# Kernel optimization log

Hardware: AMD Instinct MI355X
Metric: run time of the kernel (lower is better)

The kernel has to match this reference:

```python
import jax, jax.numpy as jnp
import numpy as np

B, T, D_MODEL, H = 2, 2048, 1024, 16
D_HEAD = D_MODEL // H


def setup_inputs() -> dict:
    key = jax.random.key(0)
    k1, k2, k3 = jax.random.split(key, 3)
    x = jax.random.normal(k1, (B, T, D_MODEL), dtype=jnp.float32)
    # Linear weights stored as (in, out); scale like torch default init roughly
    W_qkv = jax.random.normal(k2, (D_MODEL, 3 * D_MODEL), dtype=jnp.float32) / np.sqrt(D_MODEL)
    W_o = jax.random.normal(k3, (D_MODEL, D_MODEL), dtype=jnp.float32) / np.sqrt(D_MODEL)
    return {"x": x, "W_qkv": W_qkv, "W_o": W_o}


def reference(x, W_qkv, W_o):
    Bx, Tx, C = x.shape
    qkv = x @ W_qkv                                   # (B,T,3C)
    qkv = qkv.reshape(Bx, Tx, 3, H, D_HEAD)
    q = qkv[:, :, 0].transpose(0, 2, 1, 3)            # (B,H,T,D)
    k = qkv[:, :, 1].transpose(0, 2, 1, 3)
    v = qkv[:, :, 2].transpose(0, 2, 1, 3)
    scale = 1.0 / np.sqrt(D_HEAD).astype(np.float32)
    att = jnp.einsum('bhqd,bhkd->bhqk', q, k) * scale  # (B,H,T,T)
    causal = jnp.tril(jnp.ones((Tx, Tx), dtype=bool))
    att = jnp.where(causal[None, None], att, jnp.float32(-jnp.inf))
    w = jax.nn.softmax(att, axis=-1)
    out = jnp.einsum('bhqk,bhkd->bhqd', w, v)          # (B,H,T,D)
    out = out.transpose(0, 2, 1, 3).reshape(Bx, Tx, C)
    return out @ W_o
```

## Files before the change

kernel.cpp:

```cpp
#include <hip/hip_runtime.h>

typedef unsigned short u16;
typedef unsigned int u32;
typedef __bf16 bf16x8 __attribute__((ext_vector_type(8)));
typedef float f32x4 __attribute__((ext_vector_type(4)));

#define DEV __device__ __forceinline__

constexpr int BB = 2;
constexpr int TT = 2048;
constexpr int CD = 1024;
constexpr int HH = 16;
constexpr int DH = 64;
constexpr int BT = BB * TT;

#define QSCALE 0.18033688011112042f

DEV u16 f2bf(float f) {
    return __builtin_bit_cast(u16, (__bf16)f);
}

DEV f32x4 mfma16(bf16x8 a, bf16x8 b, f32x4 c) {
    return __builtin_amdgcn_mfma_f32_16x16x32_bf16(a, b, c, 0, 0, 0);
}

DEV void gld_lds16(u16* lds, const u16* g) {
    __builtin_amdgcn_global_load_lds(
        (const __attribute__((address_space(1))) unsigned int*)g,
        (__attribute__((address_space(3))) unsigned int*)lds, 16, 0, 0);
}

__global__ __launch_bounds__(256)
void prep_kernel(const float* __restrict__ x, u16* __restrict__ xb,
                 const float* __restrict__ Wqkv, u16* __restrict__ WqkvT,
                 const float* __restrict__ Wo, u16* __restrict__ WoT) {
    const int tid = threadIdx.x;
    int blk = blockIdx.x;
    if (blk < 2048) {
        const int i = (blk * 256 + tid) * 8;
        float4 a = *(const float4*)&x[i];
        float4 b = *(const float4*)&x[i + 4];
        u16 t[8];
        t[0] = f2bf(a.x); t[1] = f2bf(a.y); t[2] = f2bf(a.z); t[3] = f2bf(a.w);
        t[4] = f2bf(b.x); t[5] = f2bf(b.y); t[6] = f2bf(b.z); t[7] = f2bf(b.w);
        *(uint4*)&xb[i] = *(const uint4*)t;
        return;
    }
    __shared__ u16 tile[32][33];
    const float* in; u16* out; int rows, cols, bx, by;
    if (blk < 5120) { blk -= 2048; in = Wqkv; out = WqkvT; rows = 1024; cols = 3072; bx = blk % 96; by = blk / 96; }
    else            { blk -= 5120; in = Wo;   out = WoT;   rows = 1024; cols = 1024; bx = blk % 32; by = blk / 32; }
    const int c0 = bx * 32, r0 = by * 32;
    const int tx = tid & 31, ty = tid >> 5;
    #pragma unroll
    for (int i = ty; i < 32; i += 8)
        tile[i][tx] = f2bf(in[(r0 + i) * cols + (c0 + tx)]);
    __syncthreads();
    #pragma unroll
    for (int i = ty; i < 32; i += 8)
        out[(c0 + i) * rows + (r0 + tx)] = tile[tx][i];
}

template <int EPI, int BN, int GX>
__global__ __launch_bounds__(256)
void gemm_db(const u16* __restrict__ A, const u16* __restrict__ Bt,
             u16* __restrict__ out0, u16* __restrict__ out1,
             u16* __restrict__ out2, float* __restrict__ outf,
             int M, int N, int K) {
    constexpr int BM = 128, BK = 32, AST = 32;
    constexpr int NT = BN / 32;
    constexpr int NBLK = GX * 32;
    constexpr int CPX = NBLK / 8;
    __shared__ alignas(16) u16 As[2][BM * AST];
    __shared__ alignas(16) u16 Bs[2][BN * AST];

    const int tid  = threadIdx.x;
    const int wave = tid >> 6, lane = tid & 63;
    const int quad = lane >> 4, l16 = lane & 15;
    const int wm = (wave & 1) * 64, wn = (wave >> 1) * (BN / 2);

    int bid = (int)blockIdx.x;
    bid = (bid & 7) * CPX + (bid >> 3);
    const int bx = bid % GX, by = bid / GX;
    const int m0 = by * BM, n0 = bx * BN;

    const int srowA = wave * 32 + (lane >> 2);
    const int srowB = wave * (BN / 4) + (lane >> 2);
    const int scol  = (lane & 3) * 8;
    const u16* ga0 = A  + (size_t)(m0 + srowA) * K + scol;
    const u16* ga1 = ga0 + (size_t)16 * K;
    const u16* gb0 = Bt + (size_t)(n0 + srowB) * K + scol;
    const u16* gb1 = gb0 + (size_t)16 * K;

    auto stage = [&](int buf, int k0) {
        gld_lds16(&As[buf][wave * 1024],           ga0 + k0);
        gld_lds16(&As[buf][wave * 1024 + 512],     ga1 + k0);
        gld_lds16(&Bs[buf][wave * (BN * 8)],       gb0 + k0);
        if constexpr (BN == 128)
            gld_lds16(&Bs[buf][wave * (BN * 8) + 512], gb1 + k0);
    };

    f32x4 acc[4][NT] = {};

    stage(0, 0);
    __syncthreads();

    int cur = 0;
    for (int k0 = 0; k0 < K; k0 += BK, cur ^= 1) {
        if (k0 + BK < K) stage(cur ^ 1, k0 + BK);

        bf16x8 fa[4], fb[NT];
        #pragma unroll
        for (int mt = 0; mt < 4; ++mt)
            fa[mt] = *(const bf16x8*)&As[cur][(wm + mt * 16 + l16) * AST + quad * 8];
        #pragma unroll
        for (int nt = 0; nt < NT; ++nt)
            fb[nt] = *(const bf16x8*)&Bs[cur][(wn + nt * 16 + l16) * AST + quad * 8];
        #pragma unroll
        for (int mt = 0; mt < 4; ++mt)
            #pragma unroll
            for (int nt = 0; nt < NT; ++nt)
                acc[mt][nt] = mfma16(fa[mt], fb[nt], acc[mt][nt]);
        __syncthreads();
    }

    #pragma unroll
    for (int mt = 0; mt < 4; ++mt) {
        #pragma unroll
        for (int nt = 0; nt < NT; ++nt) {
            #pragma unroll
            for (int reg = 0; reg < 4; ++reg) {
                const int r = m0 + wm + mt * 16 + quad * 4 + reg;
                const int c = n0 + wn + nt * 16 + l16;
                if (EPI == 0) {
                    outf[(size_t)r * N + c] = acc[mt][nt][reg];
                } else {
                    const int which = c >> 10;
                    const int cc = c & 1023;
                    const int h = cc >> 6, d = cc & 63;
                    const int b = r >> 11, t = r & 2047;
                    const int bh = b * HH + h;
                    if (which == 0) {
                        out0[((size_t)bh * TT + t) * DH + d] =
                            f2bf(acc[mt][nt][reg] * QSCALE);
                    } else if (which == 1) {
                        out1[((size_t)bh * TT + t) * DH + d] = f2bf(acc[mt][nt][reg]);
                    } else {
                        out2[((size_t)bh * DH + d) * TT + t] = f2bf(acc[mt][nt][reg]);
                    }
                }
            }
        }
    }
}

constexpr int KST = 72;

DEV void attn_step(const bf16x8 fk[4][2], const bf16x8 fv[2][4],
                   const bf16x8* fq, f32x4* Oacc,
                   float& m_i, float& l_i, bool diag,
                   int wave, int quad, int l16) {
    f32x4 st[4];
    #pragma unroll
    for (int nt = 0; nt < 4; ++nt) {
        f32x4 t = {};
        t = mfma16(fk[nt][0], fq[0], t);
        t = mfma16(fk[nt][1], fq[1], t);
        st[nt] = t;
    }

    if (diag) {
        const int qg = wave * 16 + l16;
        #pragma unroll
        for (int nt = 0; nt < 4; ++nt)
            #pragma unroll
            for (int reg = 0; reg < 4; ++reg) {
                const int kg = nt * 16 + quad * 4 + reg;
                st[nt][reg] = (kg <= qg) ? st[nt][reg] : -INFINITY;
            }
    }

    float v[16];
    #pragma unroll
    for (int nt = 0; nt < 4; ++nt)
        #pragma unroll
        for (int reg = 0; reg < 4; ++reg)
            v[nt * 4 + reg] = st[nt][reg];
    #pragma unroll
    for (int s = 8; s > 0; s >>= 1)
        #pragma unroll
        for (int i = 0; i < s; ++i)
            v[i] = fmaxf(v[i], v[i + s]);
    float vmax = v[0];
    vmax = fmaxf(vmax, __shfl_xor(vmax, 16, 64));
    vmax = fmaxf(vmax, __shfl_xor(vmax, 32, 64));

    const float mnew = fmaxf(m_i, vmax);
    const float alpha = __builtin_amdgcn_exp2f(m_i - mnew);
    m_i = mnew;

    #pragma unroll
    for (int nt = 0; nt < 4; ++nt)
        #pragma unroll
        for (int reg = 0; reg < 4; ++reg) {
            const float p = __builtin_amdgcn_exp2f(st[nt][reg] - mnew);
            st[nt][reg] = p;
            v[nt * 4 + reg] = p;
        }
    #pragma unroll
    for (int s = 8; s > 0; s >>= 1)
        #pragma unroll
        for (int i = 0; i < s; ++i)
            v[i] += v[i + s];
    float vsum = v[0];
    vsum += __shfl_xor(vsum, 16, 64);
    vsum += __shfl_xor(vsum, 32, 64);
    l_i = l_i * alpha + vsum;

    #pragma unroll
    for (int dt = 0; dt < 4; ++dt)
        #pragma unroll
        for (int reg = 0; reg < 4; ++reg)
            Oacc[dt][reg] *= alpha;

    #pragma unroll
    for (int pair = 0; pair < 2; ++pair) {
        bf16x8 pb;
        #pragma unroll
        for (int j = 0; j < 4; ++j) {
            pb[j]     = (__bf16)st[2 * pair][j];
            pb[4 + j] = (__bf16)st[2 * pair + 1][j];
        }
        #pragma unroll
        for (int dt = 0; dt < 4; ++dt)
            Oacc[dt] = mfma16(fv[pair][dt], pb, Oacc[dt]);
    }
}

__global__ __launch_bounds__(256, 4)
void attn_kernel(const u16* __restrict__ Q, const u16* __restrict__ Kb,
                 const u16* __restrict__ Vt, u16* __restrict__ O) {
    __shared__ alignas(16) u16 Ks[2][64 * KST];
    __shared__ alignas(16) u16 Vs[2][64 * KST];

    const int bid = (int)blockIdx.x;
    const int j2 = bid >> 3;
    const int qt = 31 - (j2 >> 2);
    const int bh = (bid & 7) + 8 * (j2 & 3);
    const int jmax = qt;

    const int tid = threadIdx.x;
    const int wave = tid >> 6, lane = tid & 63;
    const int quad = lane >> 4, l16 = lane & 15;

    const u16* Qh = Q  + (size_t)bh * TT * DH;
    const u16* Kh = Kb + (size_t)bh * TT * DH;
    const u16* Vh = Vt + (size_t)bh * DH * TT;

    const int row = qt * 64 + wave * 16;

    bf16x8 fq[2];
    fq[0] = *(const bf16x8*)&Qh[(row + l16) * DH + quad * 8];
    fq[1] = *(const bf16x8*)&Qh[(row + l16) * DH + 32 + quad * 8];

    f32x4 Oa[4] = {};
    float m_i = -INFINITY, l_i = 0.f;

    const int trow = tid >> 3;
    const int ic   = tid & 7;
    const int tcol = ic * 8;
    const int vc1 = 32 * (ic >> 2) + 16 * (ic & 1) + 4 * ((ic & 3) >> 1);
    uint4 kr0, kr1, vr0, vr1;

    auto load_chunk = [&](int j) {
        const u16* ks = Kh + (size_t)j * 64 * DH;
        kr0 = *(const uint4*)&ks[trow * DH + tcol];
        kr1 = *(const uint4*)&ks[(trow + 32) * DH + tcol];
        const u16* vs = Vh + (size_t)j * 64;
        vr0 = *(const uint4*)&vs[(size_t)trow * TT + tcol];
        vr1 = *(const uint4*)&vs[(size_t)(trow + 32) * TT + tcol];
    };
    auto write_chunk = [&](int buf) {
        *(uint4*)&Ks[buf][trow * KST + tcol]        = kr0;
        *(uint4*)&Ks[buf][(trow + 32) * KST + tcol] = kr1;
        *(uint2*)&Vs[buf][trow * KST + vc1]            = *(const uint2*)&vr0;
        *(uint2*)&Vs[buf][trow * KST + vc1 + 8]        = *((const uint2*)&vr0 + 1);
        *(uint2*)&Vs[buf][(trow + 32) * KST + vc1]     = *(const uint2*)&vr1;
        *(uint2*)&Vs[buf][(trow + 32) * KST + vc1 + 8] = *((const uint2*)&vr1 + 1);
    };

    load_chunk(0);
    write_chunk(0);

    for (int j = 0; j <= jmax; ++j) {
        const int cur = j & 1;
        __syncthreads();
        if (j < jmax) load_chunk(j + 1);

        bf16x8 fk[4][2], fv[2][4];
        #pragma unroll
        for (int nt = 0; nt < 4; ++nt) {
            fk[nt][0] = *(const bf16x8*)&Ks[cur][(nt * 16 + l16) * KST + quad * 8];
            fk[nt][1] = *(const bf16x8*)&Ks[cur][(nt * 16 + l16) * KST + 32 + quad * 8];
        }
        #pragma unroll
        for (int pair = 0; pair < 2; ++pair)
            #pragma unroll
            for (int dt = 0; dt < 4; ++dt)
                fv[pair][dt] = *(const bf16x8*)
                    &Vs[cur][(dt * 16 + l16) * KST + pair * 32 + quad * 8];

        attn_step(fk, fv, fq, Oa, m_i, l_i, (j == qt), wave, quad, l16);
        if (j < jmax) write_chunk(cur ^ 1);
    }

    const int b = bh >> 4, h = bh & 15;
    const float r_i = 1.f / l_i;
    #pragma unroll
    for (int dt = 0; dt < 4; ++dt) {
        u16 oa[4];
        #pragma unroll
        for (int reg = 0; reg < 4; ++reg)
            oa[reg] = f2bf(Oa[dt][reg] * r_i);
        *(uint2*)&O[((size_t)(b * TT + row + l16)) * CD + h * DH + dt * 16 + quad * 4] =
            *(const uint2*)oa;
    }
}

extern "C" void kernel_launch(void* const* d_in, const int* in_sizes, int n_in,
                              void* d_out, int out_size, void* d_ws, size_t ws_size,
                              hipStream_t stream) {
    (void)in_sizes; (void)n_in; (void)out_size; (void)ws_size;
    const float* x    = (const float*)d_in[0];
    const float* Wqkv = (const float*)d_in[1];
    const float* Wo   = (const float*)d_in[2];
    float* out = (float*)d_out;

    char* ws = (char*)d_ws;
    u16* xb    = (u16*)(ws + 0);
    u16* WqkvT = (u16*)(ws + (8u  << 20));
    u16* WoT   = (u16*)(ws + (14u << 20));
    u16* Qb    = (u16*)(ws + (16u << 20));
    u16* Kb    = (u16*)(ws + (24u << 20));
    u16* Vt    = (u16*)(ws + (32u << 20));
    u16* attn  = (u16*)(ws + (40u << 20));

    prep_kernel<<<6144, 256, 0, stream>>>(x, xb, Wqkv, WqkvT, Wo, WoT);

    gemm_db<1, 128, 24><<<768, 256, 0, stream>>>(
        xb, WqkvT, Qb, Kb, Vt, nullptr, BT, 3072, CD);

    attn_kernel<<<1024, 256, 0, stream>>>(Qb, Kb, Vt, attn);

    gemm_db<0, 64, 16><<<512, 256, 0, stream>>>(
        attn, WoT, nullptr, nullptr, nullptr, out, BT, CD, CD);
}
```

Before: 177.6 us.

## Triple-buffer GEMM LDS staging with partial vmcnt waits and XOR swizzle

The GEMM mainloop moves from double to triple buffering. It prefetches two K-steps ahead and waits only on the older batch of direct-to-LDS loads, using a partial s_waitcnt vmcnt followed by a raw s_barrier in place of a full __syncthreads. This is meant to keep more global loads in flight while the MFMAs run. It also XOR-swizzles the LDS column placement to cut bank conflicts on the fragment reads. In exchange it uses 50% more LDS, which may lower occupancy, and the hardcoded vmcnt counts must match the number of loads issued per stage exactly.

```diff
diff --git a/kernel.cpp b/kernel.cpp
--- a/kernel.cpp
+++ b/kernel.cpp
@@ -71,8 +71,8 @@
     constexpr int NT = BN / 32;
     constexpr int NBLK = GX * 32;
     constexpr int CPX = NBLK / 8;
-    __shared__ alignas(16) u16 As[2][BM * AST];
-    __shared__ alignas(16) u16 Bs[2][BN * AST];
+    __shared__ alignas(16) u16 As[3][BM * AST];
+    __shared__ alignas(16) u16 Bs[3][BN * AST];
 
     const int tid  = threadIdx.x;
     const int wave = tid >> 6, lane = tid & 63;
@@ -86,7 +86,7 @@
 
     const int srowA = wave * 32 + (lane >> 2);
     const int srowB = wave * (BN / 4) + (lane >> 2);
-    const int scol  = (lane & 3) * 8;
+    const int scol  = (((lane & 3) ^ ((lane >> 3) & 3))) * 8;
     const u16* ga0 = A  + (size_t)(m0 + srowA) * K + scol;
     const u16* ga1 = ga0 + (size_t)16 * K;
     const u16* gb0 = Bt + (size_t)(n0 + srowB) * K + scol;
@@ -99,29 +99,45 @@
         if constexpr (BN == 128)
             gld_lds16(&Bs[buf][wave * (BN * 8) + 512], gb1 + k0);
     };
+    auto wait_lps = [&]() {
+        if constexpr (BN == 128) asm volatile("s_waitcnt vmcnt(4)" ::: "memory");
+        else                     asm volatile("s_waitcnt vmcnt(3)" ::: "memory");
+    };
 
     f32x4 acc[4][NT] = {};
 
     stage(0, 0);
-    __syncthreads();
-
-    int cur = 0;
-    for (int k0 = 0; k0 < K; k0 += BK, cur ^= 1) {
-        if (k0 + BK < K) stage(cur ^ 1, k0 + BK);
+    stage(1, BK);
+    wait_lps();
+    __builtin_amdgcn_s_barrier();
+
+    const int sx = ((l16 >> 1) & 3) * 8;
+    const int NS = K / BK;
+    int cb = 0;
+    for (int t = 0; t < NS; ++t) {
+        const bool pf = (t + 2 < NS);
+        int sb = cb + 2; if (sb >= 3) sb -= 3;
+        if (pf) stage(sb, (t + 2) * BK);
 
         bf16x8 fa[4], fb[NT];
         #pragma unroll
         for (int mt = 0; mt < 4; ++mt)
-            fa[mt] = *(const bf16x8*)&As[cur][(wm + mt * 16 + l16) * AST + quad * 8];
+            fa[mt] = *(const bf16x8*)
+                &As[cb][(wm + mt * 16 + l16) * AST + (quad * 8 ^ sx)];
         #pragma unroll
         for (int nt = 0; nt < NT; ++nt)
-            fb[nt] = *(const bf16x8*)&Bs[cur][(wn + nt * 16 + l16) * AST + quad * 8];
+            fb[nt] = *(const bf16x8*)
+                &Bs[cb][(wn + nt * 16 + l16) * AST + (quad * 8 ^ sx)];
         #pragma unroll
         for (int mt = 0; mt < 4; ++mt)
             #pragma unroll
             for (int nt = 0; nt < NT; ++nt)
                 acc[mt][nt] = mfma16(fa[mt], fb[nt], acc[mt][nt]);
-        __syncthreads();
+
+        if (pf) wait_lps();
+        else    asm volatile("s_waitcnt vmcnt(0)" ::: "memory");
+        __builtin_amdgcn_s_barrier();
+        cb = (cb + 1 == 3) ? 0 : cb + 1;
     }
 
     #pragma unroll
```

New measurement: 179.5 us. No clear change (+1.1%).
